# Performance work log

Hardware: AMD Instinct MI355X
Metric: run time of the kernel (lower is better)

## Reference

```python
import jax, jax.numpy as jnp
import numpy as np

B, S, D, E, H, TOPK = 4, 2048, 1024, 32, 128, 4

def setup_inputs() -> dict:
    key = jax.random.key(0)
    k1, k2, k3, k4 = jax.random.split(key, 4)
    x = jax.random.normal(k1, (B, S, D), jnp.float32)
    expert_sel = jax.random.normal(k2, (E, D), jnp.float32) * (D ** -0.5)
    keys = jax.random.normal(k3, (E, D, H), jnp.float32) * (D ** -0.5)
    values = jax.random.normal(k4, (E, H, D), jnp.float32) * (H ** -0.5)
    return {"x": x, "expert_sel": expert_sel, "keys": keys, "values": values, "n_heads": TOPK}

def reference(x, expert_sel, keys, values, n_heads):
    # x: [B,S,D]; expert_sel: [E,D]; keys: [E,D,H]; values: [E,H,D]
    Bv, Sv, Dv = x.shape
    Ev = keys.shape[0]
    xf = x.reshape(-1, Dv)                                  # [N,D]
    N = xf.shape[0]
    gate = jax.nn.sigmoid(xf @ expert_sel.T)                # [N,E] sigmoid gating (sigma-MoE)
    vals, idx = jax.lax.top_k(gate, n_heads)                # [N,k] selected experts + gate weights
    # dense per-token-per-expert gate weights; zero for non-selected experts
    g = jnp.zeros((N, Ev), x.dtype).at[jnp.arange(N)[:, None], idx].set(vals)  # [N,E]
    # grouped expert FFN, expressed densely over the (small) expert axis:
    # out = sum_e g[n,e] * relu(x @ keys[e]) @ values[e]
    h = jax.nn.relu(jnp.einsum('nd,edh->enh', xf, keys))    # [E,N,H]
    out = jnp.einsum('enh,ehd->nd', h * g.T[:, :, None], values)  # [N,D]
    return out.reshape(Bv, Sv, Dv)
```

## Files before the change

### kernel.cpp

```cpp
#include <hip/hip_runtime.h>
#include <hip/hip_bf16.h>

#define NTOK 8192
#define DDIM 1024
#define NEXP 32
#define HDIM 128
#define TOPK 4

typedef __attribute__((ext_vector_type(8))) short bf16x8;
typedef __attribute__((ext_vector_type(4))) float f32x4;

typedef unsigned int uint_g __attribute__((address_space(1)));
typedef unsigned int uint_l __attribute__((address_space(3)));

__device__ __forceinline__ void async_cp16(const void* g, void* l) {
    __builtin_amdgcn_global_load_lds((const uint_g*)g, (uint_l*)l, 16, 0, 0);
}

__device__ inline unsigned short f2bf(float f) {
    unsigned int u = __builtin_bit_cast(unsigned int, f);
    unsigned int r = (u + 0x7fffu + ((u >> 16) & 1u)) >> 16;
    return (unsigned short)r;
}
__device__ inline float bf2f(unsigned short s) {
    unsigned int u = ((unsigned int)s) << 16;
    return __builtin_bit_cast(float, u);
}

__global__ __launch_bounds__(256) void prep_gate(
    const float* __restrict__ x, const float* __restrict__ es,
    const float* __restrict__ keys, const float* __restrict__ values,
    unsigned short* __restrict__ Kb, unsigned short* __restrict__ Vb,
    unsigned short* __restrict__ Xb,
    int* __restrict__ cnt, int* __restrict__ tok_list, float* __restrict__ gates)
{
    const int tid = threadIdx.x;

    if (blockIdx.x < 4096) {
        int idx = blockIdx.x * 256 + tid;
        unsigned short o[8];
        if (idx < NEXP * 128 * 128) {
            int n = idx & 127, k0 = (idx >> 7) & 127, e = idx >> 14;
            const float* s = keys + ((size_t)e * DDIM + k0 * 8) * HDIM + n;
            #pragma unroll
            for (int j = 0; j < 8; ++j) o[j] = f2bf(s[(size_t)j * HDIM]);
            *(uint4*)&Kb[(size_t)idx * 8] = *(uint4*)o;
        } else {
            idx -= NEXP * 128 * 128;
            int n = idx & 1023, k0 = (idx >> 10) & 15, e = idx >> 14;
            const float* s = values + ((size_t)e * HDIM + k0 * 8) * DDIM + n;
            #pragma unroll
            for (int j = 0; j < 8; ++j) o[j] = f2bf(s[(size_t)j * DDIM]);
            *(uint4*)&Vb[(size_t)idx * 8] = *(uint4*)o;
        }
        return;
    }

    const int n0 = (int)(blockIdx.x - 4096) * 16;

    __shared__ float smem[4608];
    __shared__ float Ls[16 * 33];
    __shared__ int hist[NEXP];
    __shared__ int bbase[NEXP];
    float* Xt  = smem;
    float* Est = smem + 64 * 36;
    float* Lp  = smem;

    const int t4  = (tid & 3) * 4;
    const int e4  = ((tid >> 2) & 7) * 4;
    const int rep = tid >> 5;

    const int xr = tid & 15, xc4 = (tid >> 4) * 4;
    const int er = tid & 31, ec8 = (tid >> 5) * 8;

    const int ctok = tid >> 4, cd4 = (tid & 15) * 4;

    const int rtok = tid >> 5, re = tid & 31;

    float lsum[2] = {0.f, 0.f};

    if (tid < NEXP) hist[tid] = 0;

    for (int q = 0; q < 4; ++q) {
        float acc[4][4] = {};

        for (int dc = q * 256; dc < q * 256 + 256; dc += 64) {
            __syncthreads();
            {
                float4 v = *(const float4*)&x[(size_t)(n0 + xr) * DDIM + dc + xc4];
                Xt[(xc4 + 0) * 36 + xr] = v.x; Xt[(xc4 + 1) * 36 + xr] = v.y;
                Xt[(xc4 + 2) * 36 + xr] = v.z; Xt[(xc4 + 3) * 36 + xr] = v.w;
            }
            #pragma unroll
            for (int i = 0; i < 2; ++i) {
                float4 v = *(const float4*)&es[(size_t)er * DDIM + dc + ec8 + i * 4];
                Est[(ec8 + i * 4 + 0) * 36 + er] = v.x;
                Est[(ec8 + i * 4 + 1) * 36 + er] = v.y;
                Est[(ec8 + i * 4 + 2) * 36 + er] = v.z;
                Est[(ec8 + i * 4 + 3) * 36 + er] = v.w;
            }
            __syncthreads();

            {
                unsigned short o[4];
                #pragma unroll
                for (int j = 0; j < 4; ++j) o[j] = f2bf(Xt[(cd4 + j) * 36 + ctok]);
                *(uint2*)&Xb[(size_t)(n0 + ctok) * DDIM + dc + cd4] = *(uint2*)o;
            }

            #pragma unroll
            for (int s = 0; s < 8; ++s) {
                int d = s * 8 + rep;
                float4 xv = *(const float4*)&Xt[d * 36 + t4];
                float4 ev = *(const float4*)&Est[d * 36 + e4];
                const float xa[4] = {xv.x, xv.y, xv.z, xv.w};
                const float ea[4] = {ev.x, ev.y, ev.z, ev.w};
                #pragma unroll
                for (int i = 0; i < 4; ++i)
                    #pragma unroll
                    for (int j = 0; j < 4; ++j)
                        acc[i][j] = fmaf(xa[i], ea[j], acc[i][j]);
            }
        }

        __syncthreads();
        #pragma unroll
        for (int i = 0; i < 4; ++i)
            #pragma unroll
            for (int j = 0; j < 4; ++j)
                Lp[(rep * 16 + t4 + i) * 33 + e4 + j] = acc[i][j];
        __syncthreads();

        #pragma unroll
        for (int h = 0; h < 2; ++h) {
            int tok = rtok + h * 8;
            float s = 0.f;
            #pragma unroll
            for (int r = 0; r < 8; ++r) s += Lp[(r * 16 + tok) * 33 + re];
            lsum[h] += s;
        }
    }

    #pragma unroll
    for (int h = 0; h < 2; ++h) Ls[(rtok + h * 8) * 33 + re] = lsum[h];
    __syncthreads();

    int sel[TOPK]; int lpos[TOPK];
    if (tid < 16) {
        float lg[NEXP];
        #pragma unroll
        for (int e2 = 0; e2 < NEXP; ++e2) lg[e2] = Ls[tid * 33 + e2];
        float sv[TOPK];
        #pragma unroll
        for (int j = 0; j < TOPK; ++j) {
            float bv = -3.0e38f; int bi = 0;
            #pragma unroll
            for (int e2 = 0; e2 < NEXP; ++e2) {
                bool taken = false;
                #pragma unroll
                for (int q = 0; q < j; ++q) taken = taken || (sel[q] == e2);
                float v = taken ? -3.0e38f : lg[e2];
                if (v > bv) { bv = v; bi = e2; }
            }
            sel[j] = bi; sv[j] = bv;
        }
        #pragma unroll
        for (int j = 0; j < TOPK; ++j) {
            gates[(size_t)(n0 + tid) * TOPK + j] = 1.f / (1.f + expf(-sv[j]));
            lpos[j] = atomicAdd(&hist[sel[j]], 1);
        }
    }
    __syncthreads();
    if (tid < NEXP) bbase[tid] = atomicAdd(&cnt[tid], hist[tid]);
    __syncthreads();
    if (tid < 16) {
        #pragma unroll
        for (int j = 0; j < TOPK; ++j)
            tok_list[(size_t)sel[j] * NTOK + bbase[sel[j]] + lpos[j]] = (n0 + tid) * TOPK + j;
    }
}

__global__ __launch_bounds__(256) void ffn_fused(
    const unsigned short* __restrict__ Xb,
    const unsigned short* __restrict__ Kb,
    const unsigned short* __restrict__ Vb,
    const int* __restrict__ cnt, const int* __restrict__ tok_list,
    const float* __restrict__ gates,
    unsigned short* __restrict__ Ob)
{
    const int bid = blockIdx.x;
    const int e = bid & 31, tile = bid >> 5;
    const int c = cnt[e], base = tile * 64;
    if (base >= c) return;
    const int nt   = min(64, c - base);
    const int tid  = threadIdx.x, wave = tid >> 6, lane = tid & 63;
    const int lm   = lane & 15, quad = lane >> 4;
    const int r2   = (wave >> 1) * 32;
    const int c2   = (wave & 1) * 64;
    const int cw   = (wave & 1) * 32;

    __shared__ __align__(16) unsigned short KV[8192];
    __shared__ __align__(16) unsigned short XO[4608];
    __shared__ __align__(16) unsigned short Hs[64 * 140];
    __shared__ int slot[64]; __shared__ int gtok[64]; __shared__ float gs[64];

    if (tid < 64) {
        if (tid < nt) {
            int v = tok_list[(size_t)e * NTOK + base + tid];
            slot[tid] = v; gtok[tid] = v >> 2; gs[tid] = gates[v];
        } else { slot[tid] = -1; gtok[tid] = 0; gs[tid] = 0.f; }
    }
    __syncthreads();

    const unsigned short* Ke    = Kb + (size_t)e * 131072;
    const unsigned short* Ve    = Vb + (size_t)e * 131072;
    const unsigned short* xrowb = Xb + (size_t)gtok[lane] * DDIM;

    f32x4 acc[2][4];
    #pragma unroll
    for (int i = 0; i < 2; ++i)
        #pragma unroll
        for (int j = 0; j < 4; ++j) acc[i][j] = (f32x4){0.f, 0.f, 0.f, 0.f};

    auto stageA = [&](int t) {
        int dc = t * 64;
        #pragma unroll
        for (int i = 0; i < 4; ++i) {
            int p = wave * 4 + i;
            async_cp16(Ke + ((size_t)(dc / 8 + (p >> 1)) * 128 + (p & 1) * 64 + lane) * 8,
                       &KV[p * 512]);
        }
        #pragma unroll
        for (int i = 0; i < 2; ++i) {
            int k0 = wave * 2 + i;
            async_cp16(xrowb + dc + k0 * 8, &XO[k0 * 512]);
        }
    };

    stageA(0);
    __syncthreads();

    for (int t = 0; t < 16; ++t) {
        #pragma unroll
        for (int ks = 0; ks < 2; ++ks) {
            int k0 = ks * 4 + quad;
            bf16x8 a0 = *(const bf16x8*)&XO[(k0 * 64 + r2 + lm) * 8];
            bf16x8 a1 = *(const bf16x8*)&XO[(k0 * 64 + r2 + 16 + lm) * 8];
            #pragma unroll
            for (int tj = 0; tj < 4; ++tj) {
                bf16x8 bb = *(const bf16x8*)&KV[(k0 * 128 + c2 + tj * 16 + lm) * 8];
                acc[0][tj] = __builtin_amdgcn_mfma_f32_16x16x32_bf16(a0, bb, acc[0][tj], 0, 0, 0);
                acc[1][tj] = __builtin_amdgcn_mfma_f32_16x16x32_bf16(a1, bb, acc[1][tj], 0, 0, 0);
            }
        }
        if (t < 15) {
            __syncthreads();
            stageA(t + 1);
            __syncthreads();
        }
    }

    #pragma unroll
    for (int ti = 0; ti < 2; ++ti)
        #pragma unroll
        for (int reg = 0; reg < 4; ++reg) {
            int m = r2 + ti * 16 + quad * 4 + reg;
            float g = gs[m];
            #pragma unroll
            for (int tj = 0; tj < 4; ++tj)
                Hs[m * 140 + c2 + tj * 16 + lm] = f2bf(fmaxf(acc[ti][tj][reg], 0.f) * g);
        }
    __syncthreads();

    auto stageV = [&](int cc) {
        #pragma unroll
        for (int i = 0; i < 4; ++i) {
            int p = wave * 4 + i;
            async_cp16(Ve + ((size_t)p * 1024 + cc * 64 + lane) * 8, &KV[p * 512]);
        }
    };

    stageV(0);
    __syncthreads();

    const int om = tid >> 2, oq = tid & 3;
    const int os = slot[om];

    for (int cc = 0; cc < 16; ++cc) {
        f32x4 acc2[2][2];
        #pragma unroll
        for (int i = 0; i < 2; ++i) {
            acc2[i][0] = (f32x4){0.f, 0.f, 0.f, 0.f};
            acc2[i][1] = (f32x4){0.f, 0.f, 0.f, 0.f};
        }

        #pragma unroll
        for (int ks = 0; ks < 4; ++ks) {
            int k0 = ks * 4 + quad;
            bf16x8 a0 = *(const bf16x8*)&Hs[(r2 + lm) * 140 + k0 * 8];
            bf16x8 a1 = *(const bf16x8*)&Hs[(r2 + 16 + lm) * 140 + k0 * 8];
            #pragma unroll
            for (int tj = 0; tj < 2; ++tj) {
                bf16x8 bb = *(const bf16x8*)&KV[(k0 * 64 + cw + tj * 16 + lm) * 8];
                acc2[0][tj] = __builtin_amdgcn_mfma_f32_16x16x32_bf16(a0, bb, acc2[0][tj], 0, 0, 0);
                acc2[1][tj] = __builtin_amdgcn_mfma_f32_16x16x32_bf16(a1, bb, acc2[1][tj], 0, 0, 0);
            }
        }

        #pragma unroll
        for (int ti = 0; ti < 2; ++ti)
            #pragma unroll
            for (int reg = 0; reg < 4; ++reg) {
                int m = r2 + ti * 16 + quad * 4 + reg;
                XO[m * 72 + cw + lm]      = f2bf(acc2[ti][0][reg]);
                XO[m * 72 + cw + 16 + lm] = f2bf(acc2[ti][1][reg]);
            }
        __syncthreads();

        if (os >= 0) {
            uint4 v0 = *(const uint4*)&XO[om * 72 + oq * 16];
            uint4 v1 = *(const uint4*)&XO[om * 72 + oq * 16 + 8];
            unsigned short* op = Ob + (size_t)os * DDIM + cc * 64 + oq * 16;
            *(uint4*)op       = v0;
            *(uint4*)(op + 8) = v1;
        }
        if (cc < 15) stageV(cc + 1);
        __syncthreads();
    }
}

__global__ __launch_bounds__(256) void reduce_out(
    const unsigned short* __restrict__ Ob, float* __restrict__ out)
{
    const int tid = threadIdx.x;
    const int n   = blockIdx.x * 2 + (tid >> 7);
    const int cc  = (tid & 127) * 8;

    float s[8] = {};
    #pragma unroll
    for (int j = 0; j < 4; ++j) {
        uint4 v = *(const uint4*)&Ob[((size_t)n * 4 + j) * DDIM + cc];
        const unsigned int w[4] = {v.x, v.y, v.z, v.w};
        #pragma unroll
        for (int q = 0; q < 4; ++q) {
            s[q * 2 + 0] += bf2f((unsigned short)(w[q] & 0xffff));
            s[q * 2 + 1] += bf2f((unsigned short)(w[q] >> 16));
        }
    }
    float4 o0 = {s[0], s[1], s[2], s[3]};
    float4 o1 = {s[4], s[5], s[6], s[7]};
    *(float4*)&out[(size_t)n * DDIM + cc]     = o0;
    *(float4*)&out[(size_t)n * DDIM + cc + 4] = o1;
}

extern "C" void kernel_launch(void* const* d_in, const int* in_sizes, int n_in,
                              void* d_out, int out_size, void* d_ws, size_t ws_size,
                              hipStream_t stream) {
    const float* x      = (const float*)d_in[0];
    const float* es     = (const float*)d_in[1];
    const float* keys   = (const float*)d_in[2];
    const float* values = (const float*)d_in[3];
    float* out          = (float*)d_out;

    char* w = (char*)d_ws;
    int*   cnt      = (int*)w;               w += 256;
    int*   tok_list = (int*)w;               w += (size_t)NEXP * NTOK * sizeof(int);
    float* gates    = (float*)w;             w += (size_t)NTOK * TOPK * sizeof(float);
    unsigned short* Kb = (unsigned short*)w; w += (size_t)NEXP * 128 * 128 * 8 * 2;
    unsigned short* Vb = (unsigned short*)w; w += (size_t)NEXP * 16 * 1024 * 8 * 2;
    unsigned short* Xb = (unsigned short*)w; w += (size_t)NTOK * DDIM * 2;
    unsigned short* Ob = (unsigned short*)w;

    hipMemsetAsync(cnt, 0, NEXP * sizeof(int), stream);

    prep_gate<<<4096 + NTOK / 16, 256, 0, stream>>>(x, es, keys, values, Kb, Vb, Xb,
                                                    cnt, tok_list, gates);
    ffn_fused<<<128 * NEXP, 256, 0, stream>>>(Xb, Kb, Vb, cnt, tok_list, gates, Ob);
    reduce_out<<<NTOK / 2, 256, 0, stream>>>(Ob, out);
}
```

Baseline: 213.3 us.

## Halve FFN token tile to 32, prefetch gating loads, reorder prep blocks

The expert FFN kernel now handles 32 tokens per block instead of 64, doubling the grid. Each wave computes one 16-row MFMA tile, and the H fragments stay in registers across the second GEMM. The gating part of prep_gate register-prefetches the next x/expert_sel chunk before the LDS barrier, and gating blocks now get the low block indices so they are scheduled before the weight-conversion blocks. Smaller tiles should spread the uneven per-expert token counts across more CUs, at the cost of loading each expert's K/V weights twice as often.

```diff
diff --git a/kernel.cpp b/kernel.cpp
--- a/kernel.cpp
+++ b/kernel.cpp
@@ -36,8 +36,8 @@
 {
     const int tid = threadIdx.x;
 
-    if (blockIdx.x < 4096) {
-        int idx = blockIdx.x * 256 + tid;
+    if (blockIdx.x >= 512) {
+        int idx = (int)(blockIdx.x - 512) * 256 + tid;
         unsigned short o[8];
         if (idx < NEXP * 128 * 128) {
             int n = idx & 127, k0 = (idx >> 7) & 127, e = idx >> 14;
@@ -56,7 +56,7 @@
         return;
     }
 
-    const int n0 = (int)(blockIdx.x - 4096) * 16;
+    const int n0 = (int)blockIdx.x * 16;
 
     __shared__ float smem[4608];
     __shared__ float Ls[16 * 33];
@@ -81,23 +81,29 @@
 
     if (tid < NEXP) hist[tid] = 0;
 
+    float4 xv  = *(const float4*)&x[(size_t)(n0 + xr) * DDIM + xc4];
+    float4 ev0 = *(const float4*)&es[(size_t)er * DDIM + ec8];
+    float4 ev1 = *(const float4*)&es[(size_t)er * DDIM + ec8 + 4];
+
     for (int q = 0; q < 4; ++q) {
         float acc[4][4] = {};
 
-        for (int dc = q * 256; dc < q * 256 + 256; dc += 64) {
+        for (int dci = 0; dci < 4; ++dci) {
+            const int dc = q * 256 + dci * 64;
             __syncthreads();
             {
-                float4 v = *(const float4*)&x[(size_t)(n0 + xr) * DDIM + dc + xc4];
-                Xt[(xc4 + 0) * 36 + xr] = v.x; Xt[(xc4 + 1) * 36 + xr] = v.y;
-                Xt[(xc4 + 2) * 36 + xr] = v.z; Xt[(xc4 + 3) * 36 + xr] = v.w;
-            }
-            #pragma unroll
-            for (int i = 0; i < 2; ++i) {
-                float4 v = *(const float4*)&es[(size_t)er * DDIM + dc + ec8 + i * 4];
-                Est[(ec8 + i * 4 + 0) * 36 + er] = v.x;
-                Est[(ec8 + i * 4 + 1) * 36 + er] = v.y;
-                Est[(ec8 + i * 4 + 2) * 36 + er] = v.z;
-                Est[(ec8 + i * 4 + 3) * 36 + er] = v.w;
+                Xt[(xc4 + 0) * 36 + xr] = xv.x; Xt[(xc4 + 1) * 36 + xr] = xv.y;
+                Xt[(xc4 + 2) * 36 + xr] = xv.z; Xt[(xc4 + 3) * 36 + xr] = xv.w;
+                Est[(ec8 + 0) * 36 + er] = ev0.x; Est[(ec8 + 1) * 36 + er] = ev0.y;
+                Est[(ec8 + 2) * 36 + er] = ev0.z; Est[(ec8 + 3) * 36 + er] = ev0.w;
+                Est[(ec8 + 4) * 36 + er] = ev1.x; Est[(ec8 + 5) * 36 + er] = ev1.y;
+                Est[(ec8 + 6) * 36 + er] = ev1.z; Est[(ec8 + 7) * 36 + er] = ev1.w;
+            }
+            const int nxt = dc + 64;
+            if (nxt < DDIM) {
+                xv  = *(const float4*)&x[(size_t)(n0 + xr) * DDIM + nxt + xc4];
+                ev0 = *(const float4*)&es[(size_t)er * DDIM + nxt + ec8];
+                ev1 = *(const float4*)&es[(size_t)er * DDIM + nxt + ec8 + 4];
             }
             __syncthreads();
 
@@ -111,10 +117,10 @@
             #pragma unroll
             for (int s = 0; s < 8; ++s) {
                 int d = s * 8 + rep;
-                float4 xv = *(const float4*)&Xt[d * 36 + t4];
-                float4 ev = *(const float4*)&Est[d * 36 + e4];
-                const float xa[4] = {xv.x, xv.y, xv.z, xv.w};
-                const float ea[4] = {ev.x, ev.y, ev.z, ev.w};
+                float4 xa4 = *(const float4*)&Xt[d * 36 + t4];
+                float4 ea4 = *(const float4*)&Est[d * 36 + e4];
+                const float xa[4] = {xa4.x, xa4.y, xa4.z, xa4.w};
+                const float ea[4] = {ea4.x, ea4.y, ea4.z, ea4.w};
                 #pragma unroll
                 for (int i = 0; i < 4; ++i)
                     #pragma unroll
@@ -158,7 +164,7 @@
             for (int e2 = 0; e2 < NEXP; ++e2) {
                 bool taken = false;
                 #pragma unroll
-                for (int q = 0; q < j; ++q) taken = taken || (sel[q] == e2);
+                for (int qq = 0; qq < j; ++qq) taken = taken || (sel[qq] == e2);
                 float v = taken ? -3.0e38f : lg[e2];
                 if (v > bv) { bv = v; bi = e2; }
             }
@@ -190,21 +196,21 @@
 {
     const int bid = blockIdx.x;
     const int e = bid & 31, tile = bid >> 5;
-    const int c = cnt[e], base = tile * 64;
+    const int c = cnt[e], base = tile * 32;
     if (base >= c) return;
-    const int nt   = min(64, c - base);
+    const int nt   = min(32, c - base);
     const int tid  = threadIdx.x, wave = tid >> 6, lane = tid & 63;
     const int lm   = lane & 15, quad = lane >> 4;
-    const int r2   = (wave >> 1) * 32;
+    const int r2   = (wave >> 1) * 16;
     const int c2   = (wave & 1) * 64;
     const int cw   = (wave & 1) * 32;
 
     __shared__ __align__(16) unsigned short KV[8192];
-    __shared__ __align__(16) unsigned short XO[4608];
-    __shared__ __align__(16) unsigned short Hs[64 * 140];
-    __shared__ int slot[64]; __shared__ int gtok[64]; __shared__ float gs[64];
-
-    if (tid < 64) {
+    __shared__ __align__(16) unsigned short XO[2304];
+    __shared__ __align__(16) unsigned short Hs[32 * 140];
+    __shared__ int slot[32]; __shared__ int gtok[32]; __shared__ float gs[32];
+
+    if (tid < 32) {
         if (tid < nt) {
             int v = tok_list[(size_t)e * NTOK + base + tid];
             slot[tid] = v; gtok[tid] = v >> 2; gs[tid] = gates[v];
@@ -212,15 +218,13 @@
     }
     __syncthreads();
 
-    const unsigned short* Ke    = Kb + (size_t)e * 131072;
-    const unsigned short* Ve    = Vb + (size_t)e * 131072;
-    const unsigned short* xrowb = Xb + (size_t)gtok[lane] * DDIM;
-
-    f32x4 acc[2][4];
-    #pragma unroll
-    for (int i = 0; i < 2; ++i)
-        #pragma unroll
-        for (int j = 0; j < 4; ++j) acc[i][j] = (f32x4){0.f, 0.f, 0.f, 0.f};
+    const unsigned short* Ke = Kb + (size_t)e * 131072;
+    const unsigned short* Ve = Vb + (size_t)e * 131072;
+    const unsigned short* xrowb = Xb + (size_t)gtok[lane & 31] * DDIM + (lane >> 5) * 8;
+
+    f32x4 acc[4];
+    #pragma unroll
+    for (int j = 0; j < 4; ++j) acc[j] = (f32x4){0.f, 0.f, 0.f, 0.f};
 
     auto stageA = [&](int t) {
         int dc = t * 64;
@@ -230,11 +234,7 @@
             async_cp16(Ke + ((size_t)(dc / 8 + (p >> 1)) * 128 + (p & 1) * 64 + lane) * 8,
                        &KV[p * 512]);
         }
-        #pragma unroll
-        for (int i = 0; i < 2; ++i) {
-            int k0 = wave * 2 + i;
-            async_cp16(xrowb + dc + k0 * 8, &XO[k0 * 512]);
-        }
+        async_cp16(xrowb + dc + wave * 16, &XO[wave * 512]);
     };
 
     stageA(0);
@@ -244,13 +244,11 @@
         #pragma unroll
         for (int ks = 0; ks < 2; ++ks) {
             int k0 = ks * 4 + quad;
-            bf16x8 a0 = *(const bf16x8*)&XO[(k0 * 64 + r2 + lm) * 8];
-            bf16x8 a1 = *(const bf16x8*)&XO[(k0 * 64 + r2 + 16 + lm) * 8];
+            bf16x8 a0 = *(const bf16x8*)&XO[(k0 * 32 + r2 + lm) * 8];
             #pragma unroll
             for (int tj = 0; tj < 4; ++tj) {
                 bf16x8 bb = *(const bf16x8*)&KV[(k0 * 128 + c2 + tj * 16 + lm) * 8];
-                acc[0][tj] = __builtin_amdgcn_mfma_f32_16x16x32_bf16(a0, bb, acc[0][tj], 0, 0, 0);
-                acc[1][tj] = __builtin_amdgcn_mfma_f32_16x16x32_bf16(a1, bb, acc[1][tj], 0, 0, 0);
+                acc[tj] = __builtin_amdgcn_mfma_f32_16x16x32_bf16(a0, bb, acc[tj], 0, 0, 0);
             }
         }
         if (t < 15) {
@@ -261,15 +259,13 @@
     }
 
     #pragma unroll
-    for (int ti = 0; ti < 2; ++ti)
-        #pragma unroll
-        for (int reg = 0; reg < 4; ++reg) {
-            int m = r2 + ti * 16 + quad * 4 + reg;
-            float g = gs[m];
-            #pragma unroll
-            for (int tj = 0; tj < 4; ++tj)
-                Hs[m * 140 + c2 + tj * 16 + lm] = f2bf(fmaxf(acc[ti][tj][reg], 0.f) * g);
-        }
+    for (int reg = 0; reg < 4; ++reg) {
+        int m = r2 + quad * 4 + reg;
+        float g = gs[m];
+        #pragma unroll
+        for (int tj = 0; tj < 4; ++tj)
+            Hs[m * 140 + c2 + tj * 16 + lm] = f2bf(fmaxf(acc[tj][reg], 0.f) * g);
+    }
     __syncthreads();
 
     auto stageV = [&](int cc) {
@@ -283,46 +279,40 @@
     stageV(0);
     __syncthreads();
 
-    const int om = tid >> 2, oq = tid & 3;
+    bf16x8 hf[4];
+    #pragma unroll
+    for (int ks = 0; ks < 4; ++ks)
+        hf[ks] = *(const bf16x8*)&Hs[(r2 + lm) * 140 + (ks * 4 + quad) * 8];
+
+    const int om = tid >> 3, oq = tid & 7;
     const int os = slot[om];
 
     for (int cc = 0; cc < 16; ++cc) {
-        f32x4 acc2[2][2];
-        #pragma unroll
-        for (int i = 0; i < 2; ++i) {
-            acc2[i][0] = (f32x4){0.f, 0.f, 0.f, 0.f};
-            acc2[i][1] = (f32x4){0.f, 0.f, 0.f, 0.f};
-        }
+        f32x4 acc2[2];
+        acc2[0] = (f32x4){0.f, 0.f, 0.f, 0.f};
+        acc2[1] = (f32x4){0.f, 0.f, 0.f, 0.f};
 
         #pragma unroll
         for (int ks = 0; ks < 4; ++ks) {
             int k0 = ks * 4 + quad;
-            bf16x8 a0 = *(const bf16x8*)&Hs[(r2 + lm) * 140 + k0 * 8];
-            bf16x8 a1 = *(const bf16x8*)&Hs[(r2 + 16 + lm) * 140 + k0 * 8];
             #pragma unroll
             for (int tj = 0; tj < 2; ++tj) {
                 bf16x8 bb = *(const bf16x8*)&KV[(k0 * 64 + cw + tj * 16 + lm) * 8];
-                acc2[0][tj] = __builtin_amdgcn_mfma_f32_16x16x32_bf16(a0, bb, acc2[0][tj], 0, 0, 0);
-                acc2[1][tj] = __builtin_amdgcn_mfma_f32_16x16x32_bf16(a1, bb, acc2[1][tj], 0, 0, 0);
-            }
-        }
-
-        #pragma unroll
-        for (int ti = 0; ti < 2; ++ti)
-            #pragma unroll
-            for (int reg = 0; reg < 4; ++reg) {
-                int m = r2 + ti * 16 + quad * 4 + reg;
-                XO[m * 72 + cw + lm]      = f2bf(acc2[ti][0][reg]);
-                XO[m * 72 + cw + 16 + lm] = f2bf(acc2[ti][1][reg]);
-            }
+                acc2[tj] = __builtin_amdgcn_mfma_f32_16x16x32_bf16(hf[ks], bb, acc2[tj], 0, 0, 0);
+            }
+        }
+
+        #pragma unroll
+        for (int reg = 0; reg < 4; ++reg) {
+            int m = r2 + quad * 4 + reg;
+            XO[m * 72 + cw + lm]      = f2bf(acc2[0][reg]);
+            XO[m * 72 + cw + 16 + lm] = f2bf(acc2[1][reg]);
+        }
         __syncthreads();
 
         if (os >= 0) {
-            uint4 v0 = *(const uint4*)&XO[om * 72 + oq * 16];
-            uint4 v1 = *(const uint4*)&XO[om * 72 + oq * 16 + 8];
-            unsigned short* op = Ob + (size_t)os * DDIM + cc * 64 + oq * 16;
-            *(uint4*)op       = v0;
-            *(uint4*)(op + 8) = v1;
+            uint4 v0 = *(const uint4*)&XO[om * 72 + oq * 8];
+            *(uint4*)(Ob + (size_t)os * DDIM + cc * 64 + oq * 8) = v0;
         }
         if (cc < 15) stageV(cc + 1);
         __syncthreads();
@@ -373,8 +363,8 @@
 
     hipMemsetAsync(cnt, 0, NEXP * sizeof(int), stream);
 
-    prep_gate<<<4096 + NTOK / 16, 256, 0, stream>>>(x, es, keys, values, Kb, Vb, Xb,
-                                                    cnt, tok_list, gates);
-    ffn_fused<<<128 * NEXP, 256, 0, stream>>>(Xb, Kb, Vb, cnt, tok_list, gates, Ob);
+    prep_gate<<<512 + 4096, 256, 0, stream>>>(x, es, keys, values, Kb, Vb, Xb,
+                                              cnt, tok_list, gates);
+    ffn_fused<<<256 * NEXP, 256, 0, stream>>>(Xb, Kb, Vb, cnt, tok_list, gates, Ob);
     reduce_out<<<NTOK / 2, 256, 0, stream>>>(Ob, out);
 }
```

Result: faster. 197.1 us (-7.6%).
